# Kernel optimization log

Hardware: AMD Instinct MI355X
Metric: run time of the kernel (lower is better)

The kernel has to match this reference:

```python
import jax, jax.numpy as jnp
import numpy as np

WOW1 = 121  # first ring-padding window
WOW2 = 5    # second ring-padding window


def ring_windows(x, wow):
    """Circular sliding windows: [B, L, C] -> [B, L, wow*C].
    Window i covers original indices (i - (wow-1) + j) mod L, j=0..wow-1,
    matching torch cat([x[:, -wow+1:], x], 1) followed by unfold+stack."""
    B, L, C = x.shape
    idx = (jnp.arange(L)[:, None] + jnp.arange(wow)[None, :] - (wow - 1)) % L  # [L, wow]
    return x[:, idx, :].reshape(B, L, wow * C)


def _linear_params(key, fan_in, fan_out):
    k1, k2 = jax.random.split(key)
    s = 1.0 / np.sqrt(fan_in)
    W = jax.random.uniform(k1, (fan_in, fan_out), minval=-s, maxval=s, dtype=jnp.float32)
    b = jax.random.uniform(k2, (fan_out,), minval=-s, maxval=s, dtype=jnp.float32)
    return W, b


def setup_inputs() -> dict:
    key = jax.random.key(0)
    ks = jax.random.split(key, 7)
    B, L, C = 8, 4096, 4
    sps, nos = 128, 32
    x = jax.random.normal(ks[0], (B, L, C), dtype=jnp.float32)
    W0, b0 = _linear_params(ks[1], WOW1 * C, sps // 4)       # 484 -> 32
    W1, b1 = _linear_params(ks[2], sps // 4, 4 * sps)        # 32 -> 512
    Ws, bs = _linear_params(ks[3], 4 * sps, nos * sps)       # 512 -> 4096 (shared_dense_0)
    Wr, br = _linear_params(ks[4], nos * sps, 4)             # 4096 -> 4 (reshape_layer)
    W2, b2 = _linear_params(ks[5], WOW2 * 4, 8 * 4)          # 20 -> 32
    W3, b3 = _linear_params(ks[6], 8 * 4, 4)                 # 32 -> 4
    return {"x": x, "W0": W0, "b0": b0, "W1": W1, "b1": b1,
            "Ws": Ws, "bs": bs, "Wr": Wr, "br": br,
            "W2": W2, "b2": b2, "W3": W3, "b3": b3}


def reference(x, W0, b0, W1, b1, Ws, bs, Wr, br, W2, b2, W3, b3):
    h = ring_windows(x, WOW1)                 # [B, L, 484]
    h = jnp.tanh(h @ W0 + b0)                 # [B, L, sps//4]
    h = h @ W1 + b1                           # [B, L, 4*sps]
    h = h @ Ws + bs                           # [B, L, nos*sps]
    h = h @ Wr + br                           # [B, L, 4]
    h = ring_windows(h, WOW2)                 # [B, L, 20]
    h = jax.nn.relu(h @ W2 + b2)              # [B, L, 32]
    return h @ W3 + b3                        # [B, L, 4]
```

## Files before the change

kernel.cpp:

```cpp
#include <hip/hip_runtime.h>
#include <hip/hip_bf16.h>
#include <math.h>


#define L_SEQ 4096
#define TL    64

__global__ __launch_bounds__(256) void precomp1_kernel(
    const float* __restrict__ Ws, const float* __restrict__ bs,
    const float* __restrict__ Wr, float* __restrict__ T) {
  const int tid  = threadIdx.x;
  const int k    = blockIdx.x * 4 + (tid >> 6);
  const int lane = tid & 63;
  if (k >= 513) return;
  const float4* row4 = (const float4*)((k < 512) ? (Ws + (size_t)k * 4096) : bs);
  const float4* Wr4  = (const float4*)Wr;
  float a0 = 0.f, a1 = 0.f, a2 = 0.f, a3 = 0.f;
#pragma unroll 4
  for (int m4 = lane; m4 < 1024; m4 += 64) {
    const float4 rv = row4[m4];
#pragma unroll
    for (int c = 0; c < 4; ++c) {
      const float  xs = ((const float*)&rv)[c];
      const float4 w  = Wr4[m4 * 4 + c];
      a0 = fmaf(xs, w.x, a0); a1 = fmaf(xs, w.y, a1);
      a2 = fmaf(xs, w.z, a2); a3 = fmaf(xs, w.w, a3);
    }
  }
#pragma unroll
  for (int off = 32; off > 0; off >>= 1) {
    a0 += __shfl_xor(a0, off); a1 += __shfl_xor(a1, off);
    a2 += __shfl_xor(a2, off); a3 += __shfl_xor(a3, off);
  }
  if (lane == 0) {
    float4 o; o.x = a0; o.y = a1; o.z = a2; o.w = a3;
    ((float4*)T)[k] = o;
  }
}

__global__ __launch_bounds__(128) void precomp2_kernel(
    const float* __restrict__ W1, const float* __restrict__ b1,
    const float* __restrict__ br, const float* __restrict__ T,
    float* __restrict__ WcBc) {
  const int i   = blockIdx.x;
  const int t   = threadIdx.x;
  const int j   = t & 3;
  const int seg = t >> 2;
  const float4* v4 = (const float4*)((i < 32) ? (W1 + (size_t)i * 512) : b1);
  const float4* T4 = (const float4*)T;
  float acc = 0.f;
#pragma unroll
  for (int q = 0; q < 4; ++q) {
    const int m4 = seg * 4 + q;
    const float4 vv = v4[m4];
#pragma unroll
    for (int c = 0; c < 4; ++c) {
      const float4 trow = T4[m4 * 4 + c];
      acc = fmaf(((const float*)&vv)[c], ((const float*)&trow)[j], acc);
    }
  }
  __shared__ float red[128];
  red[t] = acc;
  __syncthreads();
#pragma unroll
  for (int s = 64; s >= 4; s >>= 1) {
    if (t < s) red[t] += red[t + s];
    __syncthreads();
  }
  if (t < 4) {
    float r = red[t];
    if (i == 32) r += T[512 * 4 + t] + br[t];
    WcBc[(i < 32 ? i * 4 : 128) + t] = r;
  }
}

__global__ __launch_bounds__(512) void stage1_kernel(
    const float* __restrict__ x, const float* __restrict__ W0,
    const float* __restrict__ b0, const float* __restrict__ WcBc,
    float* __restrict__ y) {
  __shared__ float4 sXv[TL + 120];
  __shared__ float4 sPre[4 * 8 * 64];
  __shared__ float4 sY2[8 * 64];

  const int b    = blockIdx.x >> 6;
  const int tile = blockIdx.x & 63;
  const int l0   = tile * TL;
  const int tid  = threadIdx.x;
  const int lane = tid & 63;

  const float4* xv = (const float4*)(x + (size_t)b * L_SEQ * 4);
  for (int i = tid; i < TL + 120; i += 512)
    sXv[i] = xv[(l0 - 120 + i) & (L_SEQ - 1)];
  __syncthreads();

  const int w  = __builtin_amdgcn_readfirstlane(tid >> 6);
  const int oh = w & 1;
  const int tc = w >> 1;
  const int d0 = tc * 30;
  const int dn = (tc < 3) ? 30 : 31;

  const float* __restrict__ Wb = W0 + oh * 16;

  float acc[16];
#pragma unroll
  for (int n = 0; n < 16; ++n) acc[n] = 0.f;

  for (int dd = 0; dd < dn; ++dd) {
    const int d = d0 + dd;
    const float4 xc = sXv[lane + d];
#pragma unroll
    for (int c = 0; c < 4; ++c) {
      const float* wr_ = Wb + (size_t)(d * 4 + c) * 32;
      const float4 w0 = *(const float4*)(wr_);
      const float4 w1 = *(const float4*)(wr_ + 4);
      const float4 w2 = *(const float4*)(wr_ + 8);
      const float4 w3 = *(const float4*)(wr_ + 12);
      const float xs = ((const float*)&xc)[c];
      acc[ 0] = fmaf(xs, w0.x, acc[ 0]); acc[ 1] = fmaf(xs, w0.y, acc[ 1]);
      acc[ 2] = fmaf(xs, w0.z, acc[ 2]); acc[ 3] = fmaf(xs, w0.w, acc[ 3]);
      acc[ 4] = fmaf(xs, w1.x, acc[ 4]); acc[ 5] = fmaf(xs, w1.y, acc[ 5]);
      acc[ 6] = fmaf(xs, w1.z, acc[ 6]); acc[ 7] = fmaf(xs, w1.w, acc[ 7]);
      acc[ 8] = fmaf(xs, w2.x, acc[ 8]); acc[ 9] = fmaf(xs, w2.y, acc[ 9]);
      acc[10] = fmaf(xs, w2.z, acc[10]); acc[11] = fmaf(xs, w2.w, acc[11]);
      acc[12] = fmaf(xs, w3.x, acc[12]); acc[13] = fmaf(xs, w3.y, acc[13]);
      acc[14] = fmaf(xs, w3.z, acc[14]); acc[15] = fmaf(xs, w3.w, acc[15]);
    }
  }

#pragma unroll
  for (int q = 0; q < 4; ++q) {
    float4 v;
    v.x = acc[q*4+0]; v.y = acc[q*4+1]; v.z = acc[q*4+2]; v.w = acc[q*4+3];
    sPre[(q * 8 + w) * 64 + lane] = v;
  }
  __syncthreads();

  {
    const int g   = w;
    const int ohg = g >> 2;
    const int qg  = g & 3;
    float4 s = sPre[(qg * 8 + (0 * 2 + ohg)) * 64 + lane];
#pragma unroll
    for (int t2 = 1; t2 < 4; ++t2) {
      const float4 p = sPre[(qg * 8 + (t2 * 2 + ohg)) * 64 + lane];
      s.x += p.x; s.y += p.y; s.z += p.z; s.w += p.w;
    }
    const float4 bb = *(const float4*)(b0 + g * 4);
    const float h0 = 1.f - 2.f / (__expf(2.f * (s.x + bb.x)) + 1.f);
    const float h1 = 1.f - 2.f / (__expf(2.f * (s.y + bb.y)) + 1.f);
    const float h2 = 1.f - 2.f / (__expf(2.f * (s.z + bb.z)) + 1.f);
    const float h3 = 1.f - 2.f / (__expf(2.f * (s.w + bb.w)) + 1.f);
    const float4 wc0 = *(const float4*)(WcBc + (4 * g + 0) * 4);
    const float4 wc1 = *(const float4*)(WcBc + (4 * g + 1) * 4);
    const float4 wc2 = *(const float4*)(WcBc + (4 * g + 2) * 4);
    const float4 wc3 = *(const float4*)(WcBc + (4 * g + 3) * 4);
    float4 yp;
    yp.x = h0*wc0.x + h1*wc1.x + h2*wc2.x + h3*wc3.x;
    yp.y = h0*wc0.y + h1*wc1.y + h2*wc2.y + h3*wc3.y;
    yp.z = h0*wc0.z + h1*wc1.z + h2*wc2.z + h3*wc3.z;
    yp.w = h0*wc0.w + h1*wc1.w + h2*wc2.w + h3*wc3.w;
    sY2[g * 64 + lane] = yp;
  }
  __syncthreads();

  if (tid < TL) {
    float4 o;
    o.x = WcBc[128 + 0]; o.y = WcBc[128 + 1];
    o.z = WcBc[128 + 2]; o.w = WcBc[128 + 3];
#pragma unroll
    for (int g2 = 0; g2 < 8; ++g2) {
      const float4 p = sY2[g2 * 64 + tid];
      o.x += p.x; o.y += p.y; o.z += p.z; o.w += p.w;
    }
    ((float4*)(y + (size_t)b * L_SEQ * 4))[l0 + tid] = o;
  }
}

__global__ __launch_bounds__(128) void stage2_kernel(
    const float* __restrict__ y, const float* __restrict__ W2,
    const float* __restrict__ b2, const float* __restrict__ W3,
    const float* __restrict__ b3, float* __restrict__ out) {
  const int g = blockIdx.x * 128 + threadIdx.x;
  const int b = g >> 12;
  const int l = g & (L_SEQ - 1);
  const float4* yv = (const float4*)(y + (size_t)b * L_SEQ * 4);

  float win[20];
#pragma unroll
  for (int j = 0; j < 5; ++j) {
    const float4 v = yv[(l - 4 + j) & (L_SEQ - 1)];
    win[j*4+0] = v.x; win[j*4+1] = v.y; win[j*4+2] = v.z; win[j*4+3] = v.w;
  }

  float h[32];
#pragma unroll
  for (int n = 0; n < 32; ++n) h[n] = b2[n];
#pragma unroll
  for (int k = 0; k < 20; ++k) {
    const float xs = win[k];
#pragma unroll
    for (int n = 0; n < 32; ++n) h[n] = fmaf(xs, W2[k*32 + n], h[n]);
  }

  float o[4];
#pragma unroll
  for (int j = 0; j < 4; ++j) o[j] = b3[j];
#pragma unroll
  for (int n = 0; n < 32; ++n) {
    const float hv = fmaxf(h[n], 0.f);
#pragma unroll
    for (int j = 0; j < 4; ++j) o[j] = fmaf(hv, W3[n*4 + j], o[j]);
  }
  float4 ov;
  ((float*)&ov)[0] = o[0]; ((float*)&ov)[1] = o[1];
  ((float*)&ov)[2] = o[2]; ((float*)&ov)[3] = o[3];
  ((float4*)out)[g] = ov;
}

extern "C" void kernel_launch(void* const* d_in, const int* in_sizes, int n_in,
                              void* d_out, int out_size, void* d_ws, size_t ws_size,
                              hipStream_t stream) {
  const float* x  = (const float*)d_in[0];
  const float* W0 = (const float*)d_in[1];
  const float* b0 = (const float*)d_in[2];
  const float* W1 = (const float*)d_in[3];
  const float* b1 = (const float*)d_in[4];
  const float* Ws = (const float*)d_in[5];
  const float* bs = (const float*)d_in[6];
  const float* Wr = (const float*)d_in[7];
  const float* br = (const float*)d_in[8];
  const float* W2 = (const float*)d_in[9];
  const float* b2 = (const float*)d_in[10];
  const float* W3 = (const float*)d_in[11];
  const float* b3 = (const float*)d_in[12];
  float* outp = (float*)d_out;

  float* T    = (float*)d_ws;
  float* WcBc = T + 2052;
  float* y    = (float*)d_ws + 2304;

  precomp1_kernel<<<129, 256, 0, stream>>>(Ws, bs, Wr, T);
  precomp2_kernel<<<33, 128, 0, stream>>>(W1, b1, br, T, WcBc);
  stage1_kernel<<<512, 512, 0, stream>>>(x, W0, b0, WcBc, y);
  stage2_kernel<<<256, 128, 0, stream>>>(y, W2, b2, W3, b3, outp);
}
```

Measured before the change: 115.7 us.

## Repartition stage1 work: 8 outputs per wave, 2 tap halves, double-buffered weights

Stage1 now splits the 121-tap window into two halves and gives each wave 8 output channels instead of 4 tap chunks × 16 channels. Weight loads are double-buffered in registers so the next tap's loads overlap the current FMAs, and launch bounds ask for 4 blocks per CU. This cuts the accumulator count and shrinks the shared-memory partial-sum reduction, aiming for higher occupancy and better latency hiding. Each wave now runs twice as many loop iterations, and the per-tap weight reads become strided float4 loads.

```diff
diff --git a/kernel.cpp b/kernel.cpp
--- a/kernel.cpp
+++ b/kernel.cpp
@@ -74,13 +74,13 @@
   }
 }
 
-__global__ __launch_bounds__(512) void stage1_kernel(
+__global__ __launch_bounds__(512, 4) void stage1_kernel(
     const float* __restrict__ x, const float* __restrict__ W0,
     const float* __restrict__ b0, const float* __restrict__ WcBc,
     float* __restrict__ y) {
   __shared__ float4 sXv[TL + 120];
-  __shared__ float4 sPre[4 * 8 * 64];
-  __shared__ float4 sY2[8 * 64];
+  __shared__ float4 sPre[16 * 64];
+  __shared__ float4 sYq[8 * 64];
 
   const int b    = blockIdx.x >> 6;
   const int tile = blockIdx.x & 63;
@@ -93,73 +93,98 @@
     sXv[i] = xv[(l0 - 120 + i) & (L_SEQ - 1)];
   __syncthreads();
 
-  const int w  = __builtin_amdgcn_readfirstlane(tid >> 6);
-  const int oh = w & 1;
-  const int tc = w >> 1;
-  const int d0 = tc * 30;
-  const int dn = (tc < 3) ? 30 : 31;
-
-  const float* __restrict__ Wb = W0 + oh * 16;
-
-  float acc[16];
-#pragma unroll
-  for (int n = 0; n < 16; ++n) acc[n] = 0.f;
-
-  for (int dd = 0; dd < dn; ++dd) {
-    const int d = d0 + dd;
-    const float4 xc = sXv[lane + d];
-#pragma unroll
-    for (int c = 0; c < 4; ++c) {
-      const float* wr_ = Wb + (size_t)(d * 4 + c) * 32;
-      const float4 w0 = *(const float4*)(wr_);
-      const float4 w1 = *(const float4*)(wr_ + 4);
-      const float4 w2 = *(const float4*)(wr_ + 8);
-      const float4 w3 = *(const float4*)(wr_ + 12);
-      const float xs = ((const float*)&xc)[c];
-      acc[ 0] = fmaf(xs, w0.x, acc[ 0]); acc[ 1] = fmaf(xs, w0.y, acc[ 1]);
-      acc[ 2] = fmaf(xs, w0.z, acc[ 2]); acc[ 3] = fmaf(xs, w0.w, acc[ 3]);
-      acc[ 4] = fmaf(xs, w1.x, acc[ 4]); acc[ 5] = fmaf(xs, w1.y, acc[ 5]);
-      acc[ 6] = fmaf(xs, w1.z, acc[ 6]); acc[ 7] = fmaf(xs, w1.w, acc[ 7]);
-      acc[ 8] = fmaf(xs, w2.x, acc[ 8]); acc[ 9] = fmaf(xs, w2.y, acc[ 9]);
-      acc[10] = fmaf(xs, w2.z, acc[10]); acc[11] = fmaf(xs, w2.w, acc[11]);
-      acc[12] = fmaf(xs, w3.x, acc[12]); acc[13] = fmaf(xs, w3.y, acc[13]);
-      acc[14] = fmaf(xs, w3.z, acc[14]); acc[15] = fmaf(xs, w3.w, acc[15]);
-    }
-  }
-
-#pragma unroll
-  for (int q = 0; q < 4; ++q) {
+  const int wu = __builtin_amdgcn_readfirstlane(tid >> 6);
+  const int th = wu & 1;
+  const int d0 = th * 60;
+  const int dn = th ? 61 : 60;
+  const int ov = (threadIdx.x >> 7) & 3;
+
+  const float4* __restrict__ W0v = (const float4*)W0;
+
+  float acc[8];
+#pragma unroll
+  for (int n = 0; n < 8; ++n) acc[n] = 0.f;
+
+#define LOADW(dst, dtap)                                            \
+  {                                                                 \
+    const int base_ = (dtap) * 32 + ov * 2;                         \
+    _Pragma("unroll")                                               \
+    for (int c_ = 0; c_ < 4; ++c_) {                                \
+      dst[c_ * 2 + 0] = W0v[base_ + c_ * 8 + 0];                    \
+      dst[c_ * 2 + 1] = W0v[base_ + c_ * 8 + 1];                    \
+    }                                                               \
+  }
+
+#define FMA8(wset, xc)                                              \
+  {                                                                 \
+    _Pragma("unroll")                                               \
+    for (int c_ = 0; c_ < 4; ++c_) {                                \
+      const float xs_ = ((const float*)&(xc))[c_];                  \
+      const float4 wq0_ = wset[c_ * 2 + 0];                         \
+      const float4 wq1_ = wset[c_ * 2 + 1];                         \
+      acc[0] = fmaf(xs_, wq0_.x, acc[0]);                           \
+      acc[1] = fmaf(xs_, wq0_.y, acc[1]);                           \
+      acc[2] = fmaf(xs_, wq0_.z, acc[2]);                           \
+      acc[3] = fmaf(xs_, wq0_.w, acc[3]);                           \
+      acc[4] = fmaf(xs_, wq1_.x, acc[4]);                           \
+      acc[5] = fmaf(xs_, wq1_.y, acc[5]);                           \
+      acc[6] = fmaf(xs_, wq1_.z, acc[6]);                           \
+      acc[7] = fmaf(xs_, wq1_.w, acc[7]);                           \
+    }                                                               \
+  }
+
+  float4 wA[8], wB[8];
+  LOADW(wA, d0);
+  float4 xcur = sXv[lane + d0];
+
+  int dd = 0;
+  for (; dd + 2 <= dn; dd += 2) {
+    const int d1   = d0 + dd + 1;
+    const bool more = (dd + 2 < dn);
+    const int d2   = more ? (d0 + dd + 2) : d0;
+    LOADW(wB, d1);
+    const float4 xn1 = sXv[lane + d1];
+    FMA8(wA, xcur);
+    LOADW(wA, d2);
+    const float4 xn2 = sXv[lane + d2];
+    FMA8(wB, xn1);
+    xcur = xn2;
+  }
+  if (dd < dn) {
+    FMA8(wA, xcur);
+  }
+#undef LOADW
+#undef FMA8
+
+#pragma unroll
+  for (int q = 0; q < 2; ++q) {
     float4 v;
     v.x = acc[q*4+0]; v.y = acc[q*4+1]; v.z = acc[q*4+2]; v.w = acc[q*4+3];
-    sPre[(q * 8 + w) * 64 + lane] = v;
+    sPre[(wu * 2 + q) * 64 + lane] = v;
   }
   __syncthreads();
 
   {
-    const int g   = w;
-    const int ohg = g >> 2;
-    const int qg  = g & 3;
-    float4 s = sPre[(qg * 8 + (0 * 2 + ohg)) * 64 + lane];
-#pragma unroll
-    for (int t2 = 1; t2 < 4; ++t2) {
-      const float4 p = sPre[(qg * 8 + (t2 * 2 + ohg)) * 64 + lane];
-      s.x += p.x; s.y += p.y; s.z += p.z; s.w += p.w;
-    }
-    const float4 bb = *(const float4*)(b0 + g * 4);
-    const float h0 = 1.f - 2.f / (__expf(2.f * (s.x + bb.x)) + 1.f);
-    const float h1 = 1.f - 2.f / (__expf(2.f * (s.y + bb.y)) + 1.f);
-    const float h2 = 1.f - 2.f / (__expf(2.f * (s.z + bb.z)) + 1.f);
-    const float h3 = 1.f - 2.f / (__expf(2.f * (s.w + bb.w)) + 1.f);
-    const float4 wc0 = *(const float4*)(WcBc + (4 * g + 0) * 4);
-    const float4 wc1 = *(const float4*)(WcBc + (4 * g + 1) * 4);
-    const float4 wc2 = *(const float4*)(WcBc + (4 * g + 2) * 4);
-    const float4 wc3 = *(const float4*)(WcBc + (4 * g + 3) * 4);
+    const int g  = wu;
+    const int o2 = g >> 1;
+    const int qq = g & 1;
+    const float4 pa = sPre[(4 * o2 + 0 + qq) * 64 + lane];
+    const float4 pb = sPre[(4 * o2 + 2 + qq) * 64 + lane];
+    const float4 bb = ((const float4*)b0)[g];
+    const float h0 = 1.f - 2.f / (__expf(2.f * (pa.x + pb.x + bb.x)) + 1.f);
+    const float h1 = 1.f - 2.f / (__expf(2.f * (pa.y + pb.y + bb.y)) + 1.f);
+    const float h2 = 1.f - 2.f / (__expf(2.f * (pa.z + pb.z + bb.z)) + 1.f);
+    const float h3 = 1.f - 2.f / (__expf(2.f * (pa.w + pb.w + bb.w)) + 1.f);
+    const float4 wc0 = ((const float4*)WcBc)[4 * g + 0];
+    const float4 wc1 = ((const float4*)WcBc)[4 * g + 1];
+    const float4 wc2 = ((const float4*)WcBc)[4 * g + 2];
+    const float4 wc3 = ((const float4*)WcBc)[4 * g + 3];
     float4 yp;
     yp.x = h0*wc0.x + h1*wc1.x + h2*wc2.x + h3*wc3.x;
     yp.y = h0*wc0.y + h1*wc1.y + h2*wc2.y + h3*wc3.y;
     yp.z = h0*wc0.z + h1*wc1.z + h2*wc2.z + h3*wc3.z;
     yp.w = h0*wc0.w + h1*wc1.w + h2*wc2.w + h3*wc3.w;
-    sY2[g * 64 + lane] = yp;
+    sYq[g * 64 + lane] = yp;
   }
   __syncthreads();
 
@@ -169,7 +194,7 @@
     o.z = WcBc[128 + 2]; o.w = WcBc[128 + 3];
 #pragma unroll
     for (int g2 = 0; g2 < 8; ++g2) {
-      const float4 p = sY2[g2 * 64 + tid];
+      const float4 p = sYq[g2 * 64 + tid];
       o.x += p.x; o.y += p.y; o.z += p.z; o.w += p.w;
     }
     ((float4*)(y + (size_t)b * L_SEQ * 4))[l0 + tid] = o;
```

New measurement: 163.3 us. +41.1%, slower.
